# Optimization experiments

Hardware: AMD Instinct MI355X
Metric: run time of the kernel (lower is better)

The kernel has to match this reference:

```python
import jax, jax.numpy as jnp
import numpy as np

BETA = 0.25


def setup_inputs() -> dict:
    key = jax.random.key(0)
    k1, k2, k3, k4 = jax.random.split(key, 4)
    n_emb, emb_dim, in_ch = 16384, 256, 1024
    feats = jax.random.normal(k1, (8, in_ch, 32, 32), dtype=jnp.float32)
    conv_w = jax.random.normal(k2, (emb_dim, in_ch), dtype=jnp.float32) * (1.0 / np.sqrt(in_ch))
    conv_b = jax.random.normal(k3, (emb_dim,), dtype=jnp.float32) * 0.01
    # torch init: uniform(-1/n_emb, 1/n_emb)
    codebook = jax.random.uniform(k4, (n_emb, emb_dim), dtype=jnp.float32,
                                  minval=-1.0 / n_emb, maxval=1.0 / n_emb)
    return {"feats": feats, "conv_w": conv_w, "conv_b": conv_b, "codebook": codebook}


def reference(feats, conv_w, conv_b, codebook):
    sg = jax.lax.stop_gradient
    # 1x1 conv == channel GEMM: [B,C,H,W] -> [B,E,H,W]
    z = jnp.einsum('bchw,ec->behw', feats, conv_w) + conv_b[None, :, None, None]
    z = jnp.transpose(z, (0, 2, 3, 1))            # [B,H,W,E]
    B, H, W, E = z.shape
    zf = z.reshape(-1, E)                          # [N,E]
    # pairwise squared distances: ||z||^2 + ||e||^2 - 2 z.e^T
    d = (jnp.sum(zf * zf, axis=1, keepdims=True)
         + jnp.sum(codebook * codebook, axis=1)
         - 2.0 * zf @ codebook.T)                  # [N,n_emb]
    idx = jnp.argmin(d, axis=1)                    # [N]
    # one-hot matmul in original == direct gather (same math)
    z_q = codebook[idx].reshape(B, H, W, E)
    loss = jnp.mean((sg(z_q) - z) ** 2) + BETA * jnp.mean((z_q - sg(z)) ** 2)
    z_q = z + sg(z_q - z)                          # straight-through
    z_q = jnp.transpose(z_q, (0, 3, 1, 2))         # [B,E,H,W]
    return (z_q, loss)
```

## Files before the change

kernel.cpp:

```cpp
#include <hip/hip_runtime.h>
#include <hip/hip_bf16.h>
#include <stdint.h>


typedef float f32x4 __attribute__((ext_vector_type(4)));
typedef int i32x4 __attribute__((ext_vector_type(4)));
typedef int i32x16 __attribute__((ext_vector_type(16)));
typedef short s16x8 __attribute__((ext_vector_type(8)));

__device__ __forceinline__ void gl2lds16(const void* g, void* l) {
  __builtin_amdgcn_global_load_lds(
      (const __attribute__((address_space(1))) void*)g,
      (__attribute__((address_space(3))) void*)l, 16, 0, 0);
}

__device__ __forceinline__ unsigned short f2bf(float f) {
  unsigned u = __float_as_uint(f);
  u = u + 0x7FFFu + ((u >> 16) & 1u);
  return (unsigned short)(u >> 16);
}

__device__ __forceinline__ ushort4 cvt4(float4 v) {
  ushort4 o;
  o.x = f2bf(v.x); o.y = f2bf(v.y); o.z = f2bf(v.z); o.w = f2bf(v.w);
  return o;
}

__global__ void k_prep(const float* __restrict__ cbk, const float* __restrict__ Wsrc,
                       signed char* __restrict__ cbs8, unsigned short* __restrict__ W2,
                       float* __restrict__ lossw, int* __restrict__ best,
                       float* __restrict__ zsq) {
  int blk = blockIdx.x, t = threadIdx.x;
  if (blk == 0 && t < 2) ((int*)lossw)[t] = 0;
  if (blk < 8) {
    #pragma unroll
    for (int k = 0; k < 4; ++k) {
      best[blk * 1024 + k * 256 + t] = (int)0x80000000;
      zsq[blk * 1024 + k * 256 + t] = 0.0f;
    }
  }
  if (blk < 256) {
    int jt = blk;
    #pragma unroll
    for (int lp = 0; lp < 4; ++lp) {
      int fl = lp * 256 + t;
      int ks = fl >> 7, fr = (fl >> 6) & 1, lane = fl & 63;
      int j = jt * 64 + fr * 32 + (lane & 31);
      int k = ks * 32 + (lane >> 5) * 16;
      const float* src = cbk + (size_t)j * 256 + k;
      int w4[4];
      #pragma unroll
      for (int q4 = 0; q4 < 4; ++q4) {
        float4 v = *(const float4*)(src + q4 * 4);
        int b0 = __float2int_rn(v.x * 2080768.0f);
        int b1 = __float2int_rn(v.y * 2080768.0f);
        int b2 = __float2int_rn(v.z * 2080768.0f);
        int b3 = __float2int_rn(v.w * 2080768.0f);
        w4[q4] = (b0 & 255) | ((b1 & 255) << 8) | ((b2 & 255) << 16) | ((b3 & 255) << 24);
      }
      int4* dst = (int4*)(cbs8 + (size_t)jt * 16384 + (size_t)fl * 16);
      *dst = make_int4(w4[0], w4[1], w4[2], w4[3]);
    }
  } else {
    size_t base = (size_t)(blk - 256) * 2048 + t * 8;
    float4 v0 = *(const float4*)(Wsrc + base);
    float4 v1 = *(const float4*)(Wsrc + base + 4);
    *(ushort4*)(W2 + base) = cvt4(v0);
    *(ushort4*)(W2 + base + 4) = cvt4(v1);
  }
}

__global__ __launch_bounds__(256, 2)
void k_gemm1(const float* __restrict__ feats, const unsigned short* __restrict__ Bw,
             const float* __restrict__ bias, signed char* __restrict__ z8,
             float* __restrict__ zsq) {
  __shared__ __align__(16) uint8_t lds[2048 * 16];
  uint8_t* ldsA = lds;
  uint8_t* ldsB = lds + 1024 * 16;
  const int t = threadIdx.x, w = t >> 6, l = t & 63;
  const int wy = w >> 1, wx = w & 1, l15 = l & 15, q = l >> 4;
  const int ib = blockIdx.y * 64, eb = blockIdx.x * 64;
  const int b1024 = (ib >> 10) * 1024, s0 = ib & 1023;
  f32x4 acc[2][2] = {};
  for (int kt = 0; kt < 8; ++kt) {
    int c0 = kt * 128;
    __syncthreads();
    #pragma unroll
    for (int r = 0; r < 8; ++r) {
      int csub = 4 * w + 16 * r;
      const float* src = feats + (size_t)(b1024 + c0 + csub) * 1024 + s0 + l;
      float4 v;
      v.x = src[0]; v.y = src[1024]; v.z = src[2048]; v.w = src[3072];
      *(ushort4*)(ldsA + ((csub >> 3) * 64 + l) * 16 + (csub & 4) * 2) = cvt4(v);
    }
    #pragma unroll
    for (int r = 0; r < 4; ++r) {
      int P = t + 256 * r;
      gl2lds16(Bw + (size_t)(eb + (P & 63)) * 1024 + c0 + (P >> 6) * 8, ldsB + P * 16);
    }
    __syncthreads();
    #pragma unroll
    for (int s = 0; s < 4; ++s) {
      s16x8 a[2], b[2];
      #pragma unroll
      for (int fr = 0; fr < 2; ++fr)
        a[fr] = *(const s16x8*)(ldsA + ((s * 4 + q) * 64 + wy * 32 + fr * 16 + l15) * 16);
      #pragma unroll
      for (int fc = 0; fc < 2; ++fc)
        b[fc] = *(const s16x8*)(ldsB + ((s * 4 + q) * 64 + wx * 32 + fc * 16 + l15) * 16);
      #pragma unroll
      for (int fr = 0; fr < 2; ++fr)
        #pragma unroll
        for (int fc = 0; fc < 2; ++fc)
          acc[fr][fc] = __builtin_amdgcn_mfma_f32_16x16x32_bf16(a[fr], b[fc], acc[fr][fc], 0, 0, 0);
    }
  }
  float zv[2][2][4];
  #pragma unroll
  for (int fc = 0; fc < 2; ++fc) {
    int e = eb + wx * 32 + fc * 16 + l15;
    float bv = bias[e];
    #pragma unroll
    for (int fr = 0; fr < 2; ++fr)
      #pragma unroll
      for (int r = 0; r < 4; ++r) {
        float zf = acc[fr][fc][r] + bv;
        zv[fc][fr][r] = zf;
        int i = ib + wy * 32 + fr * 16 + q * 4 + r;
        int qv = __float2int_rn(zf * 16.0f);
        qv = qv > 127 ? 127 : (qv < -127 ? -127 : qv);
        z8[(size_t)i * 256 + e] = (signed char)qv;
      }
  }
  #pragma unroll
  for (int fr = 0; fr < 2; ++fr)
    #pragma unroll
    for (int r = 0; r < 4; ++r) {
      float p = zv[0][fr][r] * zv[0][fr][r] + zv[1][fr][r] * zv[1][fr][r];
      p += __shfl_xor(p, 1, 64);
      p += __shfl_xor(p, 2, 64);
      p += __shfl_xor(p, 4, 64);
      p += __shfl_xor(p, 8, 64);
      if (l15 == 0)
        atomicAdd(&zsq[ib + wy * 32 + fr * 16 + q * 4 + r], p);
    }
}

__global__ __launch_bounds__(256, 2)
void k_gemm2(const signed char* __restrict__ cbs8, const signed char* __restrict__ z8,
             int* __restrict__ best) {
  __shared__ __align__(16) uint8_t ldsB[32768];
  __shared__ int csh[4][128];
  const int t = threadIdx.x, w = t >> 6, l = t & 63;
  const int l31 = l & 31, h = l >> 5;
  const int ib = blockIdx.y * 128;
  #pragma unroll
  for (int r = 0; r < 8; ++r) {
    int P = t + 256 * r;
    gl2lds16(z8 + (size_t)(ib + (P & 127)) * 256 + (P >> 7) * 16, ldsB + P * 16);
  }
  int ibest[4];
  #pragma unroll
  for (int fc = 0; fc < 4; ++fc) ibest[fc] = (int)0x80000000;
  __syncthreads();
  const uint8_t* bbase = ldsB + (h * 128 + l31) * 16;
  #pragma unroll 1
  for (int js = 0; js < 2; ++js) {
    const int jtile = blockIdx.x * 8 + js * 4 + w;
    const uint8_t* abase = (const uint8_t*)cbs8 + (size_t)jtile * 16384 + l * 16;
    i32x16 acc[2][4] = {};
    #pragma unroll 2
    for (int ks = 0; ks < 8; ++ks) {
      i32x4 a0 = *(const i32x4*)(abase + (ks * 2) * 1024);
      i32x4 a1 = *(const i32x4*)(abase + (ks * 2 + 1) * 1024);
      i32x4 b0 = *(const i32x4*)(bbase + ks * 4096);
      i32x4 b1 = *(const i32x4*)(bbase + ks * 4096 + 512);
      i32x4 b2 = *(const i32x4*)(bbase + ks * 4096 + 1024);
      i32x4 b3 = *(const i32x4*)(bbase + ks * 4096 + 1536);
      acc[0][0] = __builtin_amdgcn_mfma_i32_32x32x32_i8(a0, b0, acc[0][0], 0, 0, 0);
      acc[1][0] = __builtin_amdgcn_mfma_i32_32x32x32_i8(a1, b0, acc[1][0], 0, 0, 0);
      acc[0][1] = __builtin_amdgcn_mfma_i32_32x32x32_i8(a0, b1, acc[0][1], 0, 0, 0);
      acc[1][1] = __builtin_amdgcn_mfma_i32_32x32x32_i8(a1, b1, acc[1][1], 0, 0, 0);
      acc[0][2] = __builtin_amdgcn_mfma_i32_32x32x32_i8(a0, b2, acc[0][2], 0, 0, 0);
      acc[1][2] = __builtin_amdgcn_mfma_i32_32x32x32_i8(a1, b2, acc[1][2], 0, 0, 0);
      acc[0][3] = __builtin_amdgcn_mfma_i32_32x32x32_i8(a0, b3, acc[0][3], 0, 0, 0);
      acc[1][3] = __builtin_amdgcn_mfma_i32_32x32x32_i8(a1, b3, acc[1][3], 0, 0, 0);
    }
    const int cbase = 511 - js * 256;
    #pragma unroll
    for (int fc = 0; fc < 4; ++fc) {
      int bb = ibest[fc];
      #pragma unroll
      for (int fr = 0; fr < 2; ++fr) {
        const int c1 = cbase - fr * 32;
        #pragma unroll
        for (int rg = 0; rg < 16; rg += 2) {
          int c0 = c1 - ((rg & 3) + 8 * (rg >> 2));
          int p0 = (int)(((unsigned)acc[fr][fc][rg] << 9) + (unsigned)c0);
          int p1 = (int)(((unsigned)acc[fr][fc][rg + 1] << 9) + (unsigned)(c0 - 1));
          bb = max(max(p0, p1), bb);
        }
      }
      ibest[fc] = bb;
    }
  }
  const float inv = 1.0f / 33292288.0f;
  const int jbase = blockIdx.x * 512 + w * 64 + 4 * h;
  #pragma unroll
  for (int fc = 0; fc < 4; ++fc) {
    int p = ibest[fc];
    int accw = p >> 9;
    int loc = 511 - (p & 511);
    int j = jbase + loc;
    float s = fmaf((float)accw, inv, 3.0f);
    int gb = (int)(((unsigned)__float_as_int(s) << 14) + (unsigned)(16383 - j));
    int bb = max(gb, __shfl_xor(gb, 32, 64));
    if (l < 32) csh[w][fc * 32 + l31] = bb;
  }
  __syncthreads();
  if (t < 128) {
    int m0 = max(max(csh[0][t], csh[1][t]), max(csh[2][t], csh[3][t]));
    atomicMax(&best[ib + t], m0);
  }
}

__global__ void k_final(const float* __restrict__ cbk, const float* __restrict__ zsq,
                        const int* __restrict__ best, float* __restrict__ lossw,
                        float* __restrict__ out) {
  __shared__ float tile[32][257];
  __shared__ int lidx[32];
  int blk = blockIdx.x, t = threadIdx.x;
  int b = blk >> 5, s0 = (blk & 31) * 32;
  int gi0 = b * 1024 + s0;
  float d = 0.0f;
  if (t < 32) {
    int bv = best[gi0 + t];
    lidx[t] = 16383 - (bv & 0x3FFF);
    d = zsq[gi0 + t] - (float)(bv >> 14) * (1.0f / 1048576.0f);
  }
  if (t < 64) {
    d += __shfl_down(d, 16, 64);
    d += __shfl_down(d, 8, 64);
    d += __shfl_down(d, 4, 64);
    d += __shfl_down(d, 2, 64);
    d += __shfl_down(d, 1, 64);
  }
  if (t == 0) {
    atomicAdd(lossw, d);
    __threadfence();
    int cnt = atomicAdd((int*)lossw + 1, 1);
    if (cnt == 255) {
      __threadfence();
      float total = atomicAdd(lossw, 0.0f);
      out[2097152] = 1.25f * total * (1.0f / 2097152.0f);
    }
  }
  __syncthreads();
  int w = t >> 6, l = t & 63;
  #pragma unroll
  for (int rr = 0; rr < 8; ++rr) {
    int r = w * 8 + rr;
    const float* src = cbk + (size_t)lidx[r] * 256;
    #pragma unroll
    for (int k = 0; k < 4; ++k)
      tile[r][l + 64 * k] = src[l + 64 * k];
  }
  __syncthreads();
  int sl = t & 31, eg = t >> 5;
  size_t ob = (size_t)b * 262144 + s0 + sl;
  #pragma unroll
  for (int k = 0; k < 32; ++k) {
    int e = eg + 8 * k;
    out[ob + (size_t)e * 1024] = tile[sl][e];
  }
}

extern "C" void kernel_launch(void* const* d_in, const int* in_sizes, int n_in,
                              void* d_out, int out_size, void* d_ws, size_t ws_size,
                              hipStream_t stream) {
  const float* feats  = (const float*)d_in[0];
  const float* conv_w = (const float*)d_in[1];
  const float* conv_b = (const float*)d_in[2];
  const float* cbk    = (const float*)d_in[3];
  float* out = (float*)d_out;
  char* ws = (char*)d_ws;
  unsigned short* W2    = (unsigned short*)(ws);
  signed char*    cbs8  = (signed char*)(ws + 524288);
  signed char*    z8    = (signed char*)(ws + 4718592);
  int*            best  = (int*)(ws + 6815744);
  float*          zsq   = (float*)(ws + 6848512);
  float*          lossw = (float*)(ws + 6881280);

  k_prep<<<384, 256, 0, stream>>>(cbk, conv_w, cbs8, W2, lossw, best, zsq);
  k_gemm1<<<dim3(4, 128), 256, 0, stream>>>(feats, W2, conv_b, z8, zsq);
  k_gemm2<<<dim3(32, 64), 256, 0, stream>>>(cbs8, z8, best);
  k_final<<<256, 256, 0, stream>>>(cbk, zsq, best, lossw, out);
}
```

Before: 164.6 us.

## Fuse prep into GEMM1 and fold final gather into GEMM2 tail blocks

```diff
diff --git a/kernel.cpp b/kernel.cpp
--- a/kernel.cpp
+++ b/kernel.cpp
@@ -26,131 +26,127 @@
   return o;
 }
 
-__global__ void k_prep(const float* __restrict__ cbk, const float* __restrict__ Wsrc,
-                       signed char* __restrict__ cbs8, unsigned short* __restrict__ W2,
-                       float* __restrict__ lossw, int* __restrict__ best,
-                       float* __restrict__ zsq) {
-  int blk = blockIdx.x, t = threadIdx.x;
-  if (blk == 0 && t < 2) ((int*)lossw)[t] = 0;
-  if (blk < 8) {
-    #pragma unroll
-    for (int k = 0; k < 4; ++k) {
-      best[blk * 1024 + k * 256 + t] = (int)0x80000000;
-      zsq[blk * 1024 + k * 256 + t] = 0.0f;
-    }
-  }
-  if (blk < 256) {
-    int jt = blk;
-    #pragma unroll
-    for (int lp = 0; lp < 4; ++lp) {
-      int fl = lp * 256 + t;
-      int ks = fl >> 7, fr = (fl >> 6) & 1, lane = fl & 63;
-      int j = jt * 64 + fr * 32 + (lane & 31);
-      int k = ks * 32 + (lane >> 5) * 16;
-      const float* src = cbk + (size_t)j * 256 + k;
-      int w4[4];
-      #pragma unroll
-      for (int q4 = 0; q4 < 4; ++q4) {
-        float4 v = *(const float4*)(src + q4 * 4);
-        int b0 = __float2int_rn(v.x * 2080768.0f);
-        int b1 = __float2int_rn(v.y * 2080768.0f);
-        int b2 = __float2int_rn(v.z * 2080768.0f);
-        int b3 = __float2int_rn(v.w * 2080768.0f);
-        w4[q4] = (b0 & 255) | ((b1 & 255) << 8) | ((b2 & 255) << 16) | ((b3 & 255) << 24);
+__global__ __launch_bounds__(256, 2)
+void k_fused1(const float* __restrict__ cbk, const float* __restrict__ Wsrc,
+              const float* __restrict__ bias, const float* __restrict__ feats,
+              signed char* __restrict__ cbs8, signed char* __restrict__ z8,
+              float* __restrict__ zsq, int* __restrict__ best,
+              int* __restrict__ cnt, float* __restrict__ lossw) {
+  __shared__ __align__(16) uint8_t ldsA[4096];
+  __shared__ __align__(16) uint8_t ldsB[65536];
+  __shared__ float zs[4][16];
+  const int blk = blockIdx.x, t = threadIdx.x;
+  if (blk >= 512) {
+    if (blk < 768) {
+      int jt = blk - 512;
+      #pragma unroll
+      for (int lp = 0; lp < 4; ++lp) {
+        int fl = lp * 256 + t;
+        int ks = fl >> 7, fr = (fl >> 6) & 1, lane = fl & 63;
+        int j = jt * 64 + fr * 32 + (lane & 31);
+        int k = ks * 32 + (lane >> 5) * 16;
+        const float* src = cbk + (size_t)j * 256 + k;
+        int w4[4];
+        #pragma unroll
+        for (int q4 = 0; q4 < 4; ++q4) {
+          float4 v = *(const float4*)(src + q4 * 4);
+          int b0 = __float2int_rn(v.x * 2080768.0f);
+          int b1 = __float2int_rn(v.y * 2080768.0f);
+          int b2 = __float2int_rn(v.z * 2080768.0f);
+          int b3 = __float2int_rn(v.w * 2080768.0f);
+          w4[q4] = (b0 & 255) | ((b1 & 255) << 8) | ((b2 & 255) << 16) | ((b3 & 255) << 24);
+        }
+        *(int4*)(cbs8 + (size_t)jt * 16384 + (size_t)fl * 16) =
+            make_int4(w4[0], w4[1], w4[2], w4[3]);
       }
-      int4* dst = (int4*)(cbs8 + (size_t)jt * 16384 + (size_t)fl * 16);
-      *dst = make_int4(w4[0], w4[1], w4[2], w4[3]);
-    }
-  } else {
-    size_t base = (size_t)(blk - 256) * 2048 + t * 8;
-    float4 v0 = *(const float4*)(Wsrc + base);
-    float4 v1 = *(const float4*)(Wsrc + base + 4);
-    *(ushort4*)(W2 + base) = cvt4(v0);
-    *(ushort4*)(W2 + base + 4) = cvt4(v1);
-  }
-}
-
-__global__ __launch_bounds__(256, 2)
-void k_gemm1(const float* __restrict__ feats, const unsigned short* __restrict__ Bw,
-             const float* __restrict__ bias, signed char* __restrict__ z8,
-             float* __restrict__ zsq) {
-  __shared__ __align__(16) uint8_t lds[2048 * 16];
-  uint8_t* ldsA = lds;
-  uint8_t* ldsB = lds + 1024 * 16;
-  const int t = threadIdx.x, w = t >> 6, l = t & 63;
-  const int wy = w >> 1, wx = w & 1, l15 = l & 15, q = l >> 4;
-  const int ib = blockIdx.y * 64, eb = blockIdx.x * 64;
-  const int b1024 = (ib >> 10) * 1024, s0 = ib & 1023;
-  f32x4 acc[2][2] = {};
+    } else {
+      int bb = blk - 768;
+      #pragma unroll
+      for (int k = 0; k < 4; ++k)
+        best[bb * 1024 + k * 256 + t] = (int)0x80000000;
+      if (bb == 0) {
+        if (t < 2) ((int*)lossw)[t] = 0;
+        if (t < 64) cnt[t] = 0;
+      }
+    }
+    return;
+  }
+  const int w = t >> 6, l = t & 63, l15 = l & 15, q = l >> 4;
+  const int ib = blk * 16;
+  const int b1024 = (ib >> 10) << 10, s0 = ib & 1023;
+  const int sA = t & 15, cg = t >> 4;
+  f32x4 acc[4] = {};
   for (int kt = 0; kt < 8; ++kt) {
     int c0 = kt * 128;
     __syncthreads();
     #pragma unroll
-    for (int r = 0; r < 8; ++r) {
-      int csub = 4 * w + 16 * r;
-      const float* src = feats + (size_t)(b1024 + c0 + csub) * 1024 + s0 + l;
+    for (int r = 0; r < 2; ++r) {
+      int c = cg * 8 + r * 4;
+      const float* src = feats + (size_t)(b1024 + c0 + c) * 1024 + s0 + sA;
       float4 v;
       v.x = src[0]; v.y = src[1024]; v.z = src[2048]; v.w = src[3072];
-      *(ushort4*)(ldsA + ((csub >> 3) * 64 + l) * 16 + (csub & 4) * 2) = cvt4(v);
-    }
+      *(ushort4*)(ldsA + ((c >> 3) * 16 + sA) * 16 + (c & 4) * 2) = cvt4(v);
+    }
+    #pragma unroll
+    for (int r = 0; r < 32; ++r) {
+      int P = t + 256 * r;
+      int e = P & 255, g = P >> 8;
+      float4 v = *(const float4*)(Wsrc + (size_t)e * 1024 + c0 + g * 4);
+      *(ushort4*)(ldsB + ((g >> 1) * 256 + e) * 16 + (g & 1) * 8) = cvt4(v);
+    }
+    __syncthreads();
+    #pragma unroll
+    for (int s = 0; s < 4; ++s) {
+      s16x8 a = *(const s16x8*)(ldsA + ((s * 4 + q) * 16 + l15) * 16);
+      s16x8 b[4];
+      #pragma unroll
+      for (int fe = 0; fe < 4; ++fe)
+        b[fe] = *(const s16x8*)(ldsB + ((s * 4 + q) * 256 + w * 64 + fe * 16 + l15) * 16);
+      #pragma unroll
+      for (int fe = 0; fe < 4; ++fe)
+        acc[fe] = __builtin_amdgcn_mfma_f32_16x16x32_bf16(a, b[fe], acc[fe], 0, 0, 0);
+    }
+  }
+  float zv[4][4];
+  #pragma unroll
+  for (int fe = 0; fe < 4; ++fe) {
+    int e = w * 64 + fe * 16 + l15;
+    float bv = bias[e];
     #pragma unroll
     for (int r = 0; r < 4; ++r) {
-      int P = t + 256 * r;
-      gl2lds16(Bw + (size_t)(eb + (P & 63)) * 1024 + c0 + (P >> 6) * 8, ldsB + P * 16);
-    }
-    __syncthreads();
-    #pragma unroll
-    for (int s = 0; s < 4; ++s) {
-      s16x8 a[2], b[2];
-      #pragma unroll
-      for (int fr = 0; fr < 2; ++fr)
-        a[fr] = *(const s16x8*)(ldsA + ((s * 4 + q) * 64 + wy * 32 + fr * 16 + l15) * 16);
-      #pragma unroll
-      for (int fc = 0; fc < 2; ++fc)
-        b[fc] = *(const s16x8*)(ldsB + ((s * 4 + q) * 64 + wx * 32 + fc * 16 + l15) * 16);
-      #pragma unroll
-      for (int fr = 0; fr < 2; ++fr)
-        #pragma unroll
-        for (int fc = 0; fc < 2; ++fc)
-          acc[fr][fc] = __builtin_amdgcn_mfma_f32_16x16x32_bf16(a[fr], b[fc], acc[fr][fc], 0, 0, 0);
-    }
-  }
-  float zv[2][2][4];
-  #pragma unroll
-  for (int fc = 0; fc < 2; ++fc) {
-    int e = eb + wx * 32 + fc * 16 + l15;
-    float bv = bias[e];
-    #pragma unroll
-    for (int fr = 0; fr < 2; ++fr)
-      #pragma unroll
-      for (int r = 0; r < 4; ++r) {
-        float zf = acc[fr][fc][r] + bv;
-        zv[fc][fr][r] = zf;
-        int i = ib + wy * 32 + fr * 16 + q * 4 + r;
-        int qv = __float2int_rn(zf * 16.0f);
-        qv = qv > 127 ? 127 : (qv < -127 ? -127 : qv);
-        z8[(size_t)i * 256 + e] = (signed char)qv;
-      }
-  }
-  #pragma unroll
-  for (int fr = 0; fr < 2; ++fr)
-    #pragma unroll
-    for (int r = 0; r < 4; ++r) {
-      float p = zv[0][fr][r] * zv[0][fr][r] + zv[1][fr][r] * zv[1][fr][r];
-      p += __shfl_xor(p, 1, 64);
-      p += __shfl_xor(p, 2, 64);
-      p += __shfl_xor(p, 4, 64);
-      p += __shfl_xor(p, 8, 64);
-      if (l15 == 0)
-        atomicAdd(&zsq[ib + wy * 32 + fr * 16 + q * 4 + r], p);
-    }
+      float zf = acc[fe][r] + bv;
+      zv[fe][r] = zf;
+      int i = ib + q * 4 + r;
+      int qv = __float2int_rn(zf * 16.0f);
+      qv = qv > 127 ? 127 : (qv < -127 ? -127 : qv);
+      z8[(size_t)i * 256 + e] = (signed char)qv;
+    }
+  }
+  #pragma unroll
+  for (int r = 0; r < 4; ++r) {
+    float p = zv[0][r] * zv[0][r] + zv[1][r] * zv[1][r]
+            + zv[2][r] * zv[2][r] + zv[3][r] * zv[3][r];
+    p += __shfl_xor(p, 1, 64);
+    p += __shfl_xor(p, 2, 64);
+    p += __shfl_xor(p, 4, 64);
+    p += __shfl_xor(p, 8, 64);
+    if (l15 == 0) zs[w][q * 4 + r] = p;
+  }
+  __syncthreads();
+  if (t < 16) zsq[ib + t] = zs[0][t] + zs[1][t] + zs[2][t] + zs[3][t];
 }
 
 __global__ __launch_bounds__(256, 2)
 void k_gemm2(const signed char* __restrict__ cbs8, const signed char* __restrict__ z8,
-             int* __restrict__ best) {
-  __shared__ __align__(16) uint8_t ldsB[32768];
+             int* __restrict__ best, int* __restrict__ cnt,
+             const float* __restrict__ zsq, const float* __restrict__ cbk,
+             float* __restrict__ lossw, float* __restrict__ out) {
+  __shared__ __align__(16) uint8_t smem[32896];
   __shared__ int csh[4][128];
+  __shared__ int lidx[128];
+  __shared__ float ps[4];
+  __shared__ int tailflag;
+  uint8_t* ldsB = smem;
   const int t = threadIdx.x, w = t >> 6, l = t & 63;
   const int l31 = l & 31, h = l >> 5;
   const int ib = blockIdx.y * 128;
@@ -222,56 +218,56 @@
     int m0 = max(max(csh[0][t], csh[1][t]), max(csh[2][t], csh[3][t]));
     atomicMax(&best[ib + t], m0);
   }
-}
-
-__global__ void k_final(const float* __restrict__ cbk, const float* __restrict__ zsq,
-                        const int* __restrict__ best, float* __restrict__ lossw,
-                        float* __restrict__ out) {
-  __shared__ float tile[32][257];
-  __shared__ int lidx[32];
-  int blk = blockIdx.x, t = threadIdx.x;
-  int b = blk >> 5, s0 = (blk & 31) * 32;
-  int gi0 = b * 1024 + s0;
+  __threadfence();
+  __syncthreads();
+  if (t == 0) tailflag = (atomicAdd(&cnt[blockIdx.y], 1) == 31) ? 1 : 0;
+  __syncthreads();
+  if (!tailflag) return;
   float d = 0.0f;
-  if (t < 32) {
-    int bv = best[gi0 + t];
+  if (t < 128) {
+    int bv = atomicMax(&best[ib + t], (int)0x80000000);
     lidx[t] = 16383 - (bv & 0x3FFF);
-    d = zsq[gi0 + t] - (float)(bv >> 14) * (1.0f / 1048576.0f);
-  }
-  if (t < 64) {
-    d += __shfl_down(d, 16, 64);
-    d += __shfl_down(d, 8, 64);
-    d += __shfl_down(d, 4, 64);
-    d += __shfl_down(d, 2, 64);
-    d += __shfl_down(d, 1, 64);
-  }
+    d = zsq[ib + t] - (float)(bv >> 14) * (1.0f / 1048576.0f);
+  }
+  d += __shfl_down(d, 32, 64);
+  d += __shfl_down(d, 16, 64);
+  d += __shfl_down(d, 8, 64);
+  d += __shfl_down(d, 4, 64);
+  d += __shfl_down(d, 2, 64);
+  d += __shfl_down(d, 1, 64);
+  if (l == 0) ps[w] = d;
+  __syncthreads();
   if (t == 0) {
-    atomicAdd(lossw, d);
+    atomicAdd(lossw, ps[0] + ps[1] + ps[2] + ps[3]);
     __threadfence();
-    int cnt = atomicAdd((int*)lossw + 1, 1);
-    if (cnt == 255) {
+    int c2 = atomicAdd((int*)lossw + 1, 1);
+    if (c2 == 63) {
       __threadfence();
       float total = atomicAdd(lossw, 0.0f);
       out[2097152] = 1.25f * total * (1.0f / 2097152.0f);
     }
   }
-  __syncthreads();
-  int w = t >> 6, l = t & 63;
-  #pragma unroll
-  for (int rr = 0; rr < 8; ++rr) {
-    int r = w * 8 + rr;
-    const float* src = cbk + (size_t)lidx[r] * 256;
-    #pragma unroll
-    for (int k = 0; k < 4; ++k)
-      tile[r][l + 64 * k] = src[l + 64 * k];
-  }
-  __syncthreads();
-  int sl = t & 31, eg = t >> 5;
-  size_t ob = (size_t)b * 262144 + s0 + sl;
-  #pragma unroll
-  for (int k = 0; k < 32; ++k) {
-    int e = eg + 8 * k;
-    out[ob + (size_t)e * 1024] = tile[sl][e];
+  float (*tile)[257] = (float (*)[257])smem;
+  const int bmaj = ib >> 10, s0g = ib & 1023;
+  #pragma unroll 1
+  for (int p = 0; p < 4; ++p) {
+    __syncthreads();
+    #pragma unroll
+    for (int rr = 0; rr < 8; ++rr) {
+      int r = w * 8 + rr;
+      const float* src = cbk + (size_t)lidx[p * 32 + r] * 256;
+      #pragma unroll
+      for (int k = 0; k < 4; ++k)
+        tile[r][l + 64 * k] = src[l + 64 * k];
+    }
+    __syncthreads();
+    int sl = t & 31, eg = t >> 5;
+    size_t ob = (size_t)bmaj * 262144 + s0g + p * 32 + sl;
+    #pragma unroll
+    for (int k = 0; k < 32; ++k) {
+      int e = eg + 8 * k;
+      out[ob + (size_t)e * 1024] = tile[sl][e];
+    }
   }
 }
 
@@ -284,15 +280,15 @@
   const float* cbk    = (const float*)d_in[3];
   float* out = (float*)d_out;
   char* ws = (char*)d_ws;
-  unsigned short* W2    = (unsigned short*)(ws);
-  signed char*    cbs8  = (signed char*)(ws + 524288);
-  signed char*    z8    = (signed char*)(ws + 4718592);
-  int*            best  = (int*)(ws + 6815744);
-  float*          zsq   = (float*)(ws + 6848512);
-  float*          lossw = (float*)(ws + 6881280);
-
-  k_prep<<<384, 256, 0, stream>>>(cbk, conv_w, cbs8, W2, lossw, best, zsq);
-  k_gemm1<<<dim3(4, 128), 256, 0, stream>>>(feats, W2, conv_b, z8, zsq);
-  k_gemm2<<<dim3(32, 64), 256, 0, stream>>>(cbs8, z8, best);
-  k_final<<<256, 256, 0, stream>>>(cbk, zsq, best, lossw, out);
-}
+  signed char* cbs8  = (signed char*)(ws);
+  signed char* z8    = (signed char*)(ws + 4194304);
+  int*         best  = (int*)(ws + 6291456);
+  float*       zsq   = (float*)(ws + 6324224);
+  int*         cnt   = (int*)(ws + 6356992);
+  float*       lossw = (float*)(ws + 6357248);
+
+  k_fused1<<<776, 256, 0, stream>>>(cbk, conv_w, conv_b, feats,
+                                    cbs8, z8, zsq, best, cnt, lossw);
+  k_gemm2<<<dim3(32, 64), 256, 0, stream>>>(cbs8, z8, best, cnt,
+                                            zsq, cbk, lossw, out);
+}
```

After: 384.5 us. +133.6%, slower.
